# Optimization experiments

Hardware: AMD Instinct MI355X
Metric: run time of the kernel (lower is better)

Reference implementation:

```python
import jax, jax.numpy as jnp
import numpy as np

HEADS = 4
DIM_HEAD = 128

def setup_inputs() -> dict:
    key = jax.random.key(0)
    k1, k2, k3, k4 = jax.random.split(key, 4)
    scale = DIM_HEAD ** -0.5
    return {
        "fmap": jax.random.normal(k1, (16, 512, 32, 32), dtype=jnp.float32),
        "w_qkv": jax.random.normal(k2, (1536, 512), dtype=jnp.float32) * 0.02,
        "height": jax.random.normal(k3, (32, DIM_HEAD), dtype=jnp.float32) * scale,
        "width": jax.random.normal(k4, (32, DIM_HEAD), dtype=jnp.float32) * scale,
    }

def reference(fmap, w_qkv, height, width):
    b, c, h, w = fmap.shape
    scale = DIM_HEAD ** -0.5
    # 1x1 conv == channel GEMM: (b, 3*heads*dim_head, h, w)
    qkv = jnp.einsum('bchw,oc->bohw', fmap, w_qkv)
    # split into q,k,v and reshape to (b, heads, seq, dim_head)
    qkv = qkv.reshape(b, 3, HEADS, DIM_HEAD, h * w)
    q, k, v = (jnp.transpose(qkv[:, i], (0, 1, 3, 2)) for i in range(3))
    # content logits
    sim = jnp.einsum('bhid,bhjd->bhij', q, k) * scale
    # absolute positional bias: emb[(x,y)] = height[x] + width[y]
    emb = (height[:, None, :] + width[None, :, :]).reshape(h * w, DIM_HEAD)
    sim = sim + jnp.einsum('bhid,jd->bhij', q, emb) * scale
    attn = jax.nn.softmax(sim, axis=-1)
    out = jnp.einsum('bhij,bhjd->bhid', attn, v)  # (b, heads, seq, d)
    out = jnp.transpose(out, (0, 1, 3, 2)).reshape(b, HEADS * DIM_HEAD, h, w)
    return out
```

## Files before the change

### kernel.cpp

```cpp
#include <hip/hip_runtime.h>
#include <math.h>

#define HEADS 4
#define DIMH  128
#define NB    16
#define CIN   512
#define SEQ   1024
#define OTOT  1536
#define KQ    (CIN / 8)

typedef __attribute__((ext_vector_type(8)))  short bf16x8;
typedef __attribute__((ext_vector_type(4)))  short bf16x4;
typedef __attribute__((ext_vector_type(4)))  float f32x4;
typedef __attribute__((ext_vector_type(16))) float f32x16;

#define MFMA16(a,b,c) __builtin_amdgcn_mfma_f32_16x16x32_bf16(a,b,c,0,0,0)
#define MFMA32(a,b,c) __builtin_amdgcn_mfma_f32_32x32x16_bf16(a,b,c,0,0,0)

__device__ __forceinline__ short f2bf(float f) {
    unsigned u = __builtin_bit_cast(unsigned, f);
    u = (u + 0x7FFFu + ((u >> 16) & 1u)) >> 16;
    return (short)u;
}
__device__ __forceinline__ unsigned pk2(float lo, float hi) {
    return __builtin_amdgcn_perm(__builtin_bit_cast(unsigned, hi),
                                 __builtin_bit_cast(unsigned, lo), 0x07060302u);
}
union PF8 { unsigned u[4]; bf16x8 v; };

__global__ __launch_bounds__(256) void convert_fmap(const float* __restrict__ F,
                                                    short* __restrict__ FT2) {
    const int s  = blockIdx.x * 256 + threadIdx.x;
    const int kq = blockIdx.y, b = blockIdx.z;
    const float* src = F + ((size_t)b * CIN + kq * 8) * SEQ + s;
    float v[8];
    #pragma unroll
    for (int i = 0; i < 8; ++i) v[i] = src[(size_t)i * SEQ];
    bf16x8 pk = { f2bf(v[0]), f2bf(v[1]), f2bf(v[2]), f2bf(v[3]),
                  f2bf(v[4]), f2bf(v[5]), f2bf(v[6]), f2bf(v[7]) };
    *(bf16x8*)&FT2[(((size_t)b * KQ + kq) * SEQ + s) * 8] = pk;
}

__global__ __launch_bounds__(256) void convert_w(const float* __restrict__ W,
                                                 short* __restrict__ Wb2) {
    const int o  = blockIdx.x * 256 + threadIdx.x;
    const int kq = blockIdx.y;
    float4 v0 = *(const float4*)&W[(size_t)o * CIN + kq * 8];
    float4 v1 = *(const float4*)&W[(size_t)o * CIN + kq * 8 + 4];
    bf16x8 pk = { f2bf(v0.x), f2bf(v0.y), f2bf(v0.z), f2bf(v0.w),
                  f2bf(v1.x), f2bf(v1.y), f2bf(v1.z), f2bf(v1.w) };
    *(bf16x8*)&Wb2[((size_t)kq * OTOT + o) * 8] = pk;
}

__global__ __launch_bounds__(256, 3) void qkv_gemm(
    const short* __restrict__ Wb2, const short* __restrict__ FT2,
    const float* __restrict__ height, const float* __restrict__ width,
    short* __restrict__ Qo, short* __restrict__ Kfo, short* __restrict__ Vfo)
{
    const int L  = blockIdx.x;
    const int x8 = L & 7, m = L >> 3;
    const int g  = x8 + 8 * (m / 12);
    const int oy = m % 12;
    const int b  = g >> 3, sx = g & 7;
    const int o0 = oy * 128, s0 = sx * 128;

    const int t = threadIdx.x, l = t & 63, w = t >> 6;
    const int quad = l >> 4, ln = l & 15;
    const int wrow = (w >> 1) * 64, wcol = (w & 1) * 64;

    const short* Ap = Wb2 + (((size_t)quad * OTOT) + (o0 + wrow + ln)) * 8;
    const short* Bp = FT2 + ((((size_t)b * KQ + quad) * SEQ) + (s0 + wcol + ln)) * 8;

    f32x4 acc[4][4] = {};
    bf16x8 a0[4], b0[4], a1[4], b1[4];

#define GLOADF(ks, af, bfr) { \
    const short* ga = Ap + (size_t)(ks) * 4 * OTOT * 8; \
    const short* gb = Bp + (size_t)(ks) * 4 * SEQ * 8; \
    _Pragma("unroll") for (int i = 0; i < 4; ++i) af[i]  = *(const bf16x8*)(ga + (size_t)i * 16 * 8); \
    _Pragma("unroll") for (int j = 0; j < 4; ++j) bfr[j] = *(const bf16x8*)(gb + (size_t)j * 16 * 8); }
#define COMP(af, bfr) { \
    _Pragma("unroll") for (int i = 0; i < 4; ++i) \
        _Pragma("unroll") for (int j = 0; j < 4; ++j) \
            acc[i][j] = MFMA16(af[i], bfr[j], acc[i][j]); }

    GLOADF(0, a0, b0);
    GLOADF(1, a1, b1);
    for (int ks = 0; ks < 16; ks += 2) {
        COMP(a0, b0);
        if (ks + 2 < 16) GLOADF(ks + 2, a0, b0);
        COMP(a1, b1);
        if (ks + 3 < 16) GLOADF(ks + 3, a1, b1);
    }

    const int sec = o0 >> 9;
    const int h   = (o0 >> 7) & 3;
    const size_t bh = (size_t)b * HEADS + h;

    if (sec == 0) {
        const float qs = 0.08838834764831845f * 1.4426950408889634f;
        #pragma unroll
        for (int ti = 0; ti < 4; ++ti) {
            int d = wrow + ti * 16 + quad * 4;
            #pragma unroll
            for (int tj = 0; tj < 4; ++tj) {
                int s = s0 + wcol + tj * 16 + ln;
                f32x4 a = acc[ti][tj];
                bf16x4 pk4 = { f2bf(a[0]*qs), f2bf(a[1]*qs), f2bf(a[2]*qs), f2bf(a[3]*qs) };
                *(bf16x4*)&Qo[(bh * SEQ + s) * DIMH + d] = pk4;
            }
        }
    } else if (sec == 1) {
        #pragma unroll
        for (int ti = 0; ti < 4; ++ti) {
            int d = wrow + ti * 16 + quad * 4;
            #pragma unroll
            for (int tj = 0; tj < 4; ++tj) {
                int s = s0 + wcol + tj * 16 + ln;
                float4 hv = *(const float4*)&height[(size_t)(s >> 5) * DIMH + d];
                float4 wv = *(const float4*)&width[(size_t)(s & 31) * DIMH + d];
                f32x4 a = acc[ti][tj];
                bf16x4 pk4 = { f2bf(a[0] + hv.x + wv.x), f2bf(a[1] + hv.y + wv.y),
                               f2bf(a[2] + hv.z + wv.z), f2bf(a[3] + hv.w + wv.w) };
                *(bf16x4*)&Kfo[(((size_t)bh * 16 + (d >> 3)) * SEQ + s) * 8 + (d & 7)] = pk4;
            }
        }
    } else {
        const int slot = ((ln >> 2) & 1) * 8 + (ln & 3) + ((ln >> 3) << 2);
        #pragma unroll
        for (int ti = 0; ti < 4; ++ti) {
            int d = wrow + ti * 16 + quad * 4;
            #pragma unroll
            for (int tj = 0; tj < 4; ++tj) {
                int s = s0 + wcol + tj * 16 + ln;
                size_t vb = (((size_t)bh * 64 + (s >> 4)) * DIMH) * 16 + slot;
                f32x4 a = acc[ti][tj];
                #pragma unroll
                for (int r = 0; r < 4; ++r)
                    Vfo[vb + (size_t)(d + r) * 16] = f2bf(a[r]);
            }
        }
    }
}

#define BQ 128
#define BJ 64
#define KSTR 136

__global__ __launch_bounds__(256, 2) void attn(
    const short* __restrict__ Q, const short* __restrict__ Kf,
    const short* __restrict__ Vf, float* __restrict__ out)
{
    __shared__ short Ks[2 * BJ * KSTR];

    const int t = threadIdx.x, l = t & 63, w = t >> 6;
    const int h = l >> 5, c31 = l & 31;

    const int L = blockIdx.x;
    const int x = L & 7, inner = L >> 3;
    const int bh = x * 8 + (inner >> 3);
    const int q0 = (inner & 7) * BQ;
    const size_t obase = (size_t)bh * DIMH * SEQ;

    bf16x8 qf[8];
    {
        const short* Qp = Q + ((size_t)bh * SEQ + (q0 + w * 32 + c31)) * DIMH + h * 8;
        #pragma unroll
        for (int kc = 0; kc < 8; ++kc)
            qf[kc] = *(const bf16x8*)(Qp + kc * 16);
    }

    const short* Kg = Kf + (size_t)bh * 16 * SEQ * 8;
    const short* Vlane = Vf + (size_t)bh * 64 * (DIMH * 16) + (c31 * 16 + h * 8);

    f32x16 O[4] = {};
    float psum = 0.f;

    {
        int4 kreg[4];
        #pragma unroll
        for (int p = 0; p < 4; ++p)
            kreg[p] = *(const int4*)(Kg + ((size_t)(p * 4 + w) * SEQ + l) * 8);
        #pragma unroll
        for (int p = 0; p < 4; ++p)
            *(int4*)&Ks[l * KSTR + (p * 4 + w) * 8] = kreg[p];
    }
    __syncthreads();

    for (int ti = 0; ti < 16; ++ti) {
        const int cur = (ti & 1) * (BJ * KSTR);
        const int nxt = (BJ * KSTR) - cur;

        bf16x8 vreg[4][4];
        {
            const short* vp0 = Vlane + (size_t)(ti * 4) * (DIMH * 16);
            #pragma unroll
            for (int gi = 0; gi < 4; ++gi)
                #pragma unroll
                for (int dc = 0; dc < 4; ++dc)
                    vreg[gi][dc] = *(const bf16x8*)(vp0 + (size_t)gi * (DIMH * 16) + dc * 32 * 16);
        }
        int4 kreg[4];
        if (ti < 15) {
            const int j0n = (ti + 1) * BJ;
            #pragma unroll
            for (int p = 0; p < 4; ++p)
                kreg[p] = *(const int4*)(Kg + ((size_t)(p * 4 + w) * SEQ + j0n + l) * 8);
        }

        f32x16 S0 = {}, S1 = {};
        #pragma unroll
        for (int kc = 0; kc < 8; ++kc) {
            bf16x8 k0 = *(const bf16x8*)&Ks[cur + c31 * KSTR + kc * 16 + h * 8];
            bf16x8 k1 = *(const bf16x8*)&Ks[cur + (32 + c31) * KSTR + kc * 16 + h * 8];
            S0 = MFMA32(k0, qf[kc], S0);
            S1 = MFMA32(k1, qf[kc], S1);
        }

        #pragma unroll
        for (int half = 0; half < 2; ++half) {
            const f32x16& S = half ? S1 : S0;
            #pragma unroll
            for (int kk = 0; kk < 2; ++kk) {
                PF8 pf;
                #pragma unroll
                for (int m = 0; m < 4; ++m) {
                    float a = __builtin_amdgcn_exp2f(S[kk * 8 + 2 * m]);
                    float b = __builtin_amdgcn_exp2f(S[kk * 8 + 2 * m + 1]);
                    psum += a + b;
                    pf.u[m] = pk2(a, b);
                }
                const int gi = half * 2 + kk;
                #pragma unroll
                for (int dc = 0; dc < 4; ++dc)
                    O[dc] = MFMA32(vreg[gi][dc], pf.v, O[dc]);
            }
        }

        if (ti < 15) {
            #pragma unroll
            for (int p = 0; p < 4; ++p)
                *(int4*)&Ks[nxt + l * KSTR + (p * 4 + w) * 8] = kreg[p];
        }
        __syncthreads();
    }

    psum += __shfl_xor(psum, 32);
    float linv = 1.0f / psum;

    #pragma unroll
    for (int dc = 0; dc < 4; ++dc)
        #pragma unroll
        for (int r = 0; r < 16; ++r) {
            int d = dc * 32 + (r & 3) + 8 * (r >> 2) + 4 * h;
            out[obase + (size_t)d * SEQ + q0 + w * 32 + c31] = O[dc][r] * linv;
        }
}

extern "C" void kernel_launch(void* const* d_in, const int* in_sizes, int n_in,
                              void* d_out, int out_size, void* d_ws, size_t ws_size,
                              hipStream_t stream) {
    const float* fmap   = (const float*)d_in[0];
    const float* w_qkv  = (const float*)d_in[1];
    const float* height = (const float*)d_in[2];
    const float* width  = (const float*)d_in[3];
    float* outp = (float*)d_out;

    const size_t n_ft  = (size_t)NB * SEQ * CIN;
    const size_t n_w   = (size_t)OTOT * CIN;
    const size_t n_qkv = (size_t)NB * HEADS * SEQ * DIMH;

    short* FT2 = (short*)d_ws;
    short* Wb2 = FT2 + n_ft;
    short* Qb  = Wb2 + n_w;
    short* Kfb = Qb + n_qkv;
    short* Vfb = Kfb + n_qkv;

    convert_fmap<<<dim3(SEQ / 256, KQ, NB), 256, 0, stream>>>(fmap, FT2);
    convert_w<<<dim3(OTOT / 256, KQ), 256, 0, stream>>>(w_qkv, Wb2);
    qkv_gemm<<<dim3(8 * 12 * NB), 256, 0, stream>>>(
        Wb2, FT2, height, width, Qb, Kfb, Vfb);
    attn<<<dim3(NB * HEADS * (SEQ / BQ)), 256, 0, stream>>>(Qb, Kfb, Vfb, outp);
}
```

Baseline: 176.5 us.

## Software-pipeline attention loop and merge conversion kernels into one launch

The attention inner loop is restructured so the QK^T MFMAs for the next key tile are issued while the exp/PV MFMAs of the current tile run. The K tile is now prefetched two tiles ahead and V loads are split around the softmax work to hide latency. Separately, the fmap and weight bf16 conversion kernels are fused into a single launch with an extra z-slice for the weights, removing one kernel launch. Keeping S0/S1 live across iterations raises register pressure, and the merged grid leaves some idle blocks that exit early.

```diff
diff --git a/kernel.cpp b/kernel.cpp
--- a/kernel.cpp
+++ b/kernel.cpp
@@ -28,10 +28,23 @@
 }
 union PF8 { unsigned u[4]; bf16x8 v; };
 
-__global__ __launch_bounds__(256) void convert_fmap(const float* __restrict__ F,
-                                                    short* __restrict__ FT2) {
-    const int s  = blockIdx.x * 256 + threadIdx.x;
-    const int kq = blockIdx.y, b = blockIdx.z;
+__global__ __launch_bounds__(256) void convert_all(const float* __restrict__ F,
+                                                   const float* __restrict__ W,
+                                                   short* __restrict__ FT2,
+                                                   short* __restrict__ Wb2) {
+    const int kq = blockIdx.y;
+    if (blockIdx.z == NB) {
+        const int o = blockIdx.x * 256 + threadIdx.x;
+        float4 v0 = *(const float4*)&W[(size_t)o * CIN + kq * 8];
+        float4 v1 = *(const float4*)&W[(size_t)o * CIN + kq * 8 + 4];
+        bf16x8 pk = { f2bf(v0.x), f2bf(v0.y), f2bf(v0.z), f2bf(v0.w),
+                      f2bf(v1.x), f2bf(v1.y), f2bf(v1.z), f2bf(v1.w) };
+        *(bf16x8*)&Wb2[((size_t)kq * OTOT + o) * 8] = pk;
+        return;
+    }
+    if (blockIdx.x >= 4) return;
+    const int s = blockIdx.x * 256 + threadIdx.x;
+    const int b = blockIdx.z;
     const float* src = F + ((size_t)b * CIN + kq * 8) * SEQ + s;
     float v[8];
     #pragma unroll
@@ -39,17 +52,6 @@
     bf16x8 pk = { f2bf(v[0]), f2bf(v[1]), f2bf(v[2]), f2bf(v[3]),
                   f2bf(v[4]), f2bf(v[5]), f2bf(v[6]), f2bf(v[7]) };
     *(bf16x8*)&FT2[(((size_t)b * KQ + kq) * SEQ + s) * 8] = pk;
-}
-
-__global__ __launch_bounds__(256) void convert_w(const float* __restrict__ W,
-                                                 short* __restrict__ Wb2) {
-    const int o  = blockIdx.x * 256 + threadIdx.x;
-    const int kq = blockIdx.y;
-    float4 v0 = *(const float4*)&W[(size_t)o * CIN + kq * 8];
-    float4 v1 = *(const float4*)&W[(size_t)o * CIN + kq * 8 + 4];
-    bf16x8 pk = { f2bf(v0.x), f2bf(v0.y), f2bf(v0.z), f2bf(v0.w),
-                  f2bf(v1.x), f2bf(v1.y), f2bf(v1.z), f2bf(v1.w) };
-    *(bf16x8*)&Wb2[((size_t)kq * OTOT + o) * 8] = pk;
 }
 
 __global__ __launch_bounds__(256, 3) void qkv_gemm(
@@ -147,6 +149,53 @@
 #define BJ 64
 #define KSTR 136
 
+#define ATTN_ITER(ti, DO_QK, DO_PRE, DO_BAR)                                        \
+{                                                                                   \
+    const int rd = (((ti) + 1) & 1) * (BJ * KSTR);                                  \
+    const int wr = ((ti) & 1) * (BJ * KSTR);                                        \
+    const short* vp0 = Vlane + (size_t)((ti) * 4) * (DIMH * 16);                    \
+    bf16x8 vr[4][4];                                                                \
+    _Pragma("unroll") for (int gi = 0; gi < 2; ++gi)                                \
+      _Pragma("unroll") for (int dc = 0; dc < 4; ++dc)                              \
+        vr[gi][dc] = *(const bf16x8*)(vp0 + (size_t)gi * (DIMH * 16) + dc * 32 * 16);\
+    int4 kreg[4];                                                                   \
+    if (DO_PRE) {                                                                   \
+        _Pragma("unroll") for (int p = 0; p < 4; ++p)                               \
+            kreg[p] = *(const int4*)(Kg + ((size_t)(p * 4 + w) * SEQ + ((ti) + 2) * BJ + l) * 8); \
+    }                                                                               \
+    PF8 pf[4];                                                                      \
+    _Pragma("unroll") for (int g = 0; g < 4; ++g) {                                 \
+        const f32x16& Sh = (g & 2) ? S1 : S0;                                       \
+        const int kk = g & 1;                                                       \
+        _Pragma("unroll") for (int mm = 0; mm < 4; ++mm) {                          \
+            float ea = __builtin_amdgcn_exp2f(Sh[kk * 8 + 2 * mm]);                 \
+            float eb = __builtin_amdgcn_exp2f(Sh[kk * 8 + 2 * mm + 1]);             \
+            psum += ea + eb;                                                        \
+            pf[g].u[mm] = pk2(ea, eb);                                              \
+        }                                                                           \
+    }                                                                               \
+    _Pragma("unroll") for (int gi = 2; gi < 4; ++gi)                                \
+      _Pragma("unroll") for (int dc = 0; dc < 4; ++dc)                              \
+        vr[gi][dc] = *(const bf16x8*)(vp0 + (size_t)gi * (DIMH * 16) + dc * 32 * 16);\
+    if (DO_QK) {                                                                    \
+        S0 = (f32x16){}; S1 = (f32x16){};                                           \
+        _Pragma("unroll") for (int kc = 0; kc < 8; ++kc) {                          \
+            bf16x8 k0 = *(const bf16x8*)&Ks[rd + c31 * KSTR + kc * 16 + h * 8];     \
+            bf16x8 k1 = *(const bf16x8*)&Ks[rd + (32 + c31) * KSTR + kc * 16 + h * 8]; \
+            S0 = MFMA32(k0, qf[kc], S0);                                            \
+            S1 = MFMA32(k1, qf[kc], S1);                                            \
+        }                                                                           \
+    }                                                                               \
+    _Pragma("unroll") for (int g = 0; g < 4; ++g)                                   \
+        _Pragma("unroll") for (int dc = 0; dc < 4; ++dc)                            \
+            O[dc] = MFMA32(vr[g][dc], pf[g].v, O[dc]);                              \
+    if (DO_PRE) {                                                                   \
+        _Pragma("unroll") for (int p = 0; p < 4; ++p)                               \
+            *(int4*)&Ks[wr + l * KSTR + (p * 4 + w) * 8] = kreg[p];                 \
+    }                                                                               \
+    if (DO_BAR) __syncthreads();                                                    \
+}
+
 __global__ __launch_bounds__(256, 2) void attn(
     const short* __restrict__ Q, const short* __restrict__ Kf,
     const short* __restrict__ Vf, float* __restrict__ out)
@@ -177,73 +226,37 @@
     float psum = 0.f;
 
     {
-        int4 kreg[4];
-        #pragma unroll
-        for (int p = 0; p < 4; ++p)
-            kreg[p] = *(const int4*)(Kg + ((size_t)(p * 4 + w) * SEQ + l) * 8);
-        #pragma unroll
-        for (int p = 0; p < 4; ++p)
-            *(int4*)&Ks[l * KSTR + (p * 4 + w) * 8] = kreg[p];
+        int4 k0[4], k1[4];
+        #pragma unroll
+        for (int p = 0; p < 4; ++p) {
+            k0[p] = *(const int4*)(Kg + ((size_t)(p * 4 + w) * SEQ + l) * 8);
+            k1[p] = *(const int4*)(Kg + ((size_t)(p * 4 + w) * SEQ + BJ + l) * 8);
+        }
+        #pragma unroll
+        for (int p = 0; p < 4; ++p) {
+            *(int4*)&Ks[l * KSTR + (p * 4 + w) * 8] = k0[p];
+            *(int4*)&Ks[BJ * KSTR + l * KSTR + (p * 4 + w) * 8] = k1[p];
+        }
     }
     __syncthreads();
 
-    for (int ti = 0; ti < 16; ++ti) {
-        const int cur = (ti & 1) * (BJ * KSTR);
-        const int nxt = (BJ * KSTR) - cur;
-
-        bf16x8 vreg[4][4];
-        {
-            const short* vp0 = Vlane + (size_t)(ti * 4) * (DIMH * 16);
-            #pragma unroll
-            for (int gi = 0; gi < 4; ++gi)
-                #pragma unroll
-                for (int dc = 0; dc < 4; ++dc)
-                    vreg[gi][dc] = *(const bf16x8*)(vp0 + (size_t)gi * (DIMH * 16) + dc * 32 * 16);
-        }
-        int4 kreg[4];
-        if (ti < 15) {
-            const int j0n = (ti + 1) * BJ;
-            #pragma unroll
-            for (int p = 0; p < 4; ++p)
-                kreg[p] = *(const int4*)(Kg + ((size_t)(p * 4 + w) * SEQ + j0n + l) * 8);
-        }
-
-        f32x16 S0 = {}, S1 = {};
-        #pragma unroll
-        for (int kc = 0; kc < 8; ++kc) {
-            bf16x8 k0 = *(const bf16x8*)&Ks[cur + c31 * KSTR + kc * 16 + h * 8];
-            bf16x8 k1 = *(const bf16x8*)&Ks[cur + (32 + c31) * KSTR + kc * 16 + h * 8];
-            S0 = MFMA32(k0, qf[kc], S0);
-            S1 = MFMA32(k1, qf[kc], S1);
-        }
-
-        #pragma unroll
-        for (int half = 0; half < 2; ++half) {
-            const f32x16& S = half ? S1 : S0;
-            #pragma unroll
-            for (int kk = 0; kk < 2; ++kk) {
-                PF8 pf;
-                #pragma unroll
-                for (int m = 0; m < 4; ++m) {
-                    float a = __builtin_amdgcn_exp2f(S[kk * 8 + 2 * m]);
-                    float b = __builtin_amdgcn_exp2f(S[kk * 8 + 2 * m + 1]);
-                    psum += a + b;
-                    pf.u[m] = pk2(a, b);
-                }
-                const int gi = half * 2 + kk;
-                #pragma unroll
-                for (int dc = 0; dc < 4; ++dc)
-                    O[dc] = MFMA32(vreg[gi][dc], pf.v, O[dc]);
-            }
-        }
-
-        if (ti < 15) {
-            #pragma unroll
-            for (int p = 0; p < 4; ++p)
-                *(int4*)&Ks[nxt + l * KSTR + (p * 4 + w) * 8] = kreg[p];
-        }
-        __syncthreads();
-    }
+    f32x16 S0 = {}, S1 = {};
+    #pragma unroll
+    for (int kc = 0; kc < 8; ++kc) {
+        bf16x8 k0 = *(const bf16x8*)&Ks[c31 * KSTR + kc * 16 + h * 8];
+        bf16x8 k1 = *(const bf16x8*)&Ks[(32 + c31) * KSTR + kc * 16 + h * 8];
+        S0 = MFMA32(k0, qf[kc], S0);
+        S1 = MFMA32(k1, qf[kc], S1);
+    }
+    __syncthreads();
+
+    for (int p = 0; p < 7; ++p) {
+        const int t0 = 2 * p;
+        ATTN_ITER(t0,     true, true, true);
+        ATTN_ITER(t0 + 1, true, true, true);
+    }
+    ATTN_ITER(14, true,  false, false);
+    ATTN_ITER(15, false, false, false);
 
     psum += __shfl_xor(psum, 32);
     float linv = 1.0f / psum;
@@ -276,8 +289,7 @@
     short* Kfb = Qb + n_qkv;
     short* Vfb = Kfb + n_qkv;
 
-    convert_fmap<<<dim3(SEQ / 256, KQ, NB), 256, 0, stream>>>(fmap, FT2);
-    convert_w<<<dim3(OTOT / 256, KQ), 256, 0, stream>>>(w_qkv, Wb2);
+    convert_all<<<dim3(6, KQ, NB + 1), 256, 0, stream>>>(fmap, w_qkv, FT2, Wb2);
     qkv_gemm<<<dim3(8 * 12 * NB), 256, 0, stream>>>(
         Wb2, FT2, height, width, Qb, Kfb, Vfb);
     attn<<<dim3(NB * HEADS * (SEQ / BQ)), 256, 0, stream>>>(Qb, Kfb, Vfb, outp);
```

After: 172.1 us. -2.5%, faster.
